# Performance work log

Hardware: AMD Instinct MI355X
Metric: run time of the kernel (lower is better)

Reference implementation:

```python
import jax, jax.numpy as jnp
import numpy as np

V, E, CIN, COUT, NH, HID = 8192, 2048, 128, 128, 4, 32
EPS = 1e-5

def _ln(x, g, b):
    m = x.mean(-1, keepdims=True)
    v = x.var(-1, keepdims=True)
    return (x - m) / jnp.sqrt(v + EPS) * g + b

def setup_inputs() -> dict:
    key = jax.random.key(0)
    ks = jax.random.split(key, 12)
    s = 0.05
    X = jax.random.normal(ks[0], (V, CIN), jnp.float32)
    H = jax.random.bernoulli(ks[1], 0.02, (V, E)).astype(jnp.float32)
    edge_features = jax.random.normal(ks[2], (E, COUT), jnp.float32)
    Wv = jax.random.normal(ks[3], (CIN, COUT), jnp.float32) * s
    bv = jnp.zeros((COUT,), jnp.float32)
    We = jax.random.normal(ks[4], (COUT, COUT), jnp.float32) * s
    be = jnp.zeros((COUT,), jnp.float32)
    vW1 = jax.random.normal(ks[5], (NH, CIN, HID), jnp.float32) * s
    vb1 = jnp.zeros((NH, HID), jnp.float32)
    vW2 = jax.random.normal(ks[6], (NH, HID), jnp.float32) * s
    vb2 = jnp.zeros((NH,), jnp.float32)
    eW1 = jax.random.normal(ks[7], (COUT, HID), jnp.float32) * s
    eb1 = jnp.zeros((HID,), jnp.float32)
    eW2 = jax.random.normal(ks[8], (HID,), jnp.float32) * s
    eb2 = jnp.zeros((), jnp.float32)
    Wc = jax.random.normal(ks[9], (NH * COUT, COUT), jnp.float32) * s
    bc = jnp.zeros((COUT,), jnp.float32)
    Wg = jax.random.normal(ks[10], (CIN + COUT, COUT), jnp.float32) * s
    bg = jnp.zeros((COUT,), jnp.float32)
    return dict(X=X, H=H, edge_features=edge_features, Wv=Wv, bv=bv, We=We, be=be,
                vW1=vW1, vb1=vb1, vW2=vW2, vb2=vb2, eW1=eW1, eb1=eb1, eW2=eW2, eb2=eb2,
                Wc=Wc, bc=bc,
                ln_e_g=jnp.ones((COUT,), jnp.float32), ln_e_b=jnp.zeros((COUT,), jnp.float32),
                ln_v_g=jnp.ones((COUT,), jnp.float32), ln_v_b=jnp.zeros((COUT,), jnp.float32),
                bn_g=jnp.ones((COUT,), jnp.float32), bn_b=jnp.zeros((COUT,), jnp.float32),
                Wg=Wg, bg=bg)

def reference(X, H, edge_features, Wv, bv, We, be, vW1, vb1, vW2, vb2,
              eW1, eb1, eW2, eb2, Wc, bc, ln_e_g, ln_e_b, ln_v_g, ln_v_b,
              bn_g, bn_b, Wg, bg):
    gelu = lambda t: jax.nn.gelu(t, approximate=False)  # torch nn.GELU default (erf)
    Ht = H.T                                   # (E, V)
    Xt = X @ Wv + bv                           # (V, Cout) theta_v
    # per-head vertex attention MLP: Linear(Cin,32)->GELU->Linear(32,1), vectorized over heads
    hid = gelu(jnp.einsum('vc,hck->hvk', X, vW1) + vb1[:, None, :])
    attn = jax.nn.sigmoid(jnp.einsum('hvk,hk->hv', hid, vW2) + vb2[:, None])  # (NH, V)
    deg = Ht.sum(axis=1, keepdims=True)        # (E, 1) edge degrees
    denom = jnp.maximum(deg, 1.0)
    # degree-normalized attention-weighted v2e aggregation per head
    head_e = jnp.einsum('ev,hvc->hec', Ht, Xt[None] * attn[:, :, None]) / denom[None]
    e_cat = jnp.transpose(head_e, (1, 0, 2)).reshape(E, NH * COUT)  # concat heads dim=1
    e_feat = e_cat @ Wc + bc                   # attn_combine
    # edge attention uses the LAST head's vertex weights (global-var quirk in torch code)
    edge_att = ((Ht @ attn[-1]) / jnp.maximum(deg[:, 0], 1.0))[:, None]  # (E,1)
    # edge-feature gating with e_attention head 0
    te = edge_features @ We + be               # theta_e
    e_scores = gelu(e_feat @ eW1 + eb1) @ eW2 + eb2
    ew = jax.nn.sigmoid(e_scores)[:, None]
    e_feat = e_feat * ew + te * (1.0 - ew)
    # normalize == 'both': layer_norm_e then batch_norm (training-mode batch stats)
    e_feat = _ln(e_feat, ln_e_g, ln_e_b)
    m = e_feat.mean(axis=0)
    v = e_feat.var(axis=0)
    e_feat = (e_feat - m) / jnp.sqrt(v + EPS) * bn_g + bn_b
    # e2v sum aggregation: H @ e_feat
    v_feat = H @ e_feat                        # (V, Cout)
    gate = jax.nn.sigmoid(jnp.concatenate([X, v_feat], axis=1) @ Wg + bg)
    v_feat = gate * v_feat + (1.0 - gate) * Xt
    v_feat = _ln(v_feat, ln_v_g, ln_v_b)
    v_feat = v_feat + X                        # residual (Cin == Cout)
    v_feat = gelu(v_feat)                      # not is_last: activation; dropout = identity (eval)
    e_feat = gelu(e_feat)
    return v_feat, e_feat, edge_att
```

## Files before the change

### kernel.cpp

```cpp
#include <hip/hip_runtime.h>
#include <hip/hip_bf16.h>
#include <math.h>

#define NV 8192
#define NE 2048
#define CIN 128
#define COUT 128
#define NH 4
#define HID 32
#define EPB 4
#define LCAP 256
#define VCAP 96
#define NWORDS (NE / 64)
#define TWORDS (NV / 64)
#define EPSV 1e-5f

__device__ __forceinline__ float gelu_f(float x) {
    return 0.5f * x * (1.0f + erff(x * 0.70710678118654752f));
}
__device__ __forceinline__ float sigmoid_f(float x) {
    return 1.0f / (1.0f + expf(-x));
}

__global__ __launch_bounds__(128) void k_vertex1(
    const float* __restrict__ X, const float* __restrict__ Wv, const float* __restrict__ bv,
    const float* __restrict__ vW1, const float* __restrict__ vb1,
    const float* __restrict__ vW2, const float* __restrict__ vb2,
    float* __restrict__ Xt, float* __restrict__ attn4)
{
    const int VPB = 8;
    __shared__ float Xs[VPB][CIN];
    int t = threadIdx.x;
    int v0 = blockIdx.x * VPB;
    for (int v = 0; v < VPB; ++v) Xs[v][t] = X[(v0 + v) * CIN + t];
    __syncthreads();

    float acc[VPB];
    float bvc = bv[t];
#pragma unroll
    for (int v = 0; v < VPB; ++v) acc[v] = bvc;
    for (int k = 0; k < CIN; ++k) {
        float w = Wv[k * COUT + t];
#pragma unroll
        for (int v = 0; v < VPB; ++v) acc[v] = fmaf(Xs[v][k], w, acc[v]);
    }
    for (int v = 0; v < VPB; ++v) Xt[(v0 + v) * COUT + t] = acc[v];

    int h = t >> 5, j = t & 31;
    float hb = vb1[h * HID + j];
#pragma unroll
    for (int v = 0; v < VPB; ++v) acc[v] = hb;
    for (int k = 0; k < CIN; ++k) {
        float w = vW1[(h * CIN + k) * HID + j];
#pragma unroll
        for (int v = 0; v < VPB; ++v) acc[v] = fmaf(Xs[v][k], w, acc[v]);
    }
    float w2 = vW2[h * HID + j];
    float b2 = vb2[h];
    for (int v = 0; v < VPB; ++v) {
        float val = gelu_f(acc[v]) * w2;
#pragma unroll
        for (int m = 16; m >= 1; m >>= 1) val += __shfl_xor(val, m, 64);
        if (j == 0) attn4[(v0 + v) * NH + h] = sigmoid_f(val + b2);
    }
}

__global__ __launch_bounds__(256) void k_build(
    const float* __restrict__ H, unsigned long long* __restrict__ Hbits,
    int* __restrict__ vdeg, int* __restrict__ vlist)
{
    int w = threadIdx.x >> 6;
    int lane = threadIdx.x & 63;
    int v = blockIdx.x * 4 + w;
    const float* row = H + (size_t)v * NE;
    unsigned long long lt = (1ull << lane) - 1ull;
    int base = 0;
    int* vl = vlist + (size_t)v * VCAP;
#pragma unroll 8
    for (int it = 0; it < NWORDS; ++it) {
        float hv = row[it * 64 + lane];
        bool nz = hv != 0.0f;
        unsigned long long m = __ballot(nz);
        if (lane == 0) Hbits[(size_t)v * NWORDS + it] = m;
        if (nz) {
            int pos = base + __popcll(m & lt);
            if (pos < VCAP) vl[pos] = it * 64 + lane;
        }
        base += __popcll(m);
    }
    if (lane == 0) vdeg[v] = base;
}

__global__ __launch_bounds__(256) void k_transpose(
    const unsigned long long* __restrict__ Hbits, unsigned long long* __restrict__ HbitsT)
{
    __shared__ unsigned long long rows[64][NWORDS];
    int t = threadIdx.x;
    int vt = blockIdx.x;
    for (int i = t; i < 64 * NWORDS; i += 256)
        rows[i >> 5][i & 31] = Hbits[(size_t)vt * 64 * NWORDS + i];
    __syncthreads();
    int wv = t >> 6;
    int lane = t & 63;
    const unsigned long long M[6] = {
        0xFFFFFFFF00000000ULL, 0xFFFF0000FFFF0000ULL, 0xFF00FF00FF00FF00ULL,
        0xF0F0F0F0F0F0F0F0ULL, 0xCCCCCCCCCCCCCCCCULL, 0xAAAAAAAAAAAAAAAAULL };
    const int js[6] = {32, 16, 8, 4, 2, 1};
#pragma unroll
    for (int itb = 0; itb < 8; ++itb) {
        int it = wv * 8 + itb;
        unsigned long long x = rows[lane][it];
#pragma unroll
        for (int s = 0; s < 6; ++s) {
            int j = js[s];
            unsigned long long y = __shfl_xor(x, j, 64);
            unsigned long long Ms = M[s];
            if ((lane & j) == 0) x = (x & ~Ms) | ((y << j) & Ms);
            else                 x = (x & Ms) | ((y >> j) & ~Ms);
        }
        HbitsT[(size_t)(it * 64 + lane) * TWORDS + vt] = x;
    }
}

__global__ __launch_bounds__(512) void k_edge(
    const float* __restrict__ Xt, const float* __restrict__ attn4,
    const unsigned long long* __restrict__ HbitsT,
    const float* __restrict__ edge_features,
    const float* __restrict__ Wc, const float* __restrict__ bc,
    const float* __restrict__ We, const float* __restrict__ be,
    const float* __restrict__ eW1, const float* __restrict__ eb1,
    const float* __restrict__ eW2, const float* __restrict__ eb2,
    const float* __restrict__ ln_g, const float* __restrict__ ln_b,
    float* __restrict__ e_ln, float* __restrict__ out_att)
{
    __shared__ int lst[EPB][LCAP];
    __shared__ int wsum[EPB][2];
    __shared__ float ecat[EPB][NH * COUT];
    __shared__ float efpart[4][EPB * COUT];
    __shared__ float tepart[4][EPB * COUT];
    __shared__ float efr_s[EPB][COUT];
    __shared__ float efs[EPB][COUT];
    __shared__ float teL[EPB][COUT];
    __shared__ float ews[EPB];
    __shared__ float red[EPB][2][2];

    int t = threadIdx.x;
    int g = t >> 7;
    int c = t & 127;
    int lane = t & 63;
    int gw = (t >> 6) & 1;
    int e0 = blockIdx.x * EPB;
    int e = e0 + g;

    efr_s[g][c] = edge_features[(size_t)e * COUT + c];

    unsigned long long wd = HbitsT[(size_t)e * TWORDS + c];
    int cntT = __popcll(wd);
    int inc = cntT;
#pragma unroll
    for (int s = 1; s < 64; s <<= 1) {
        int y = __shfl_up(inc, s, 64);
        if (lane >= s) inc += y;
    }
    if (lane == 63) wsum[g][gw] = inc;
    __syncthreads();
    int base = (gw ? wsum[g][0] : 0) + inc - cntT;
    int n0 = wsum[g][0] + wsum[g][1];
    int vbase = c * 64;
    unsigned long long mm = wd;
    while (mm) {
        int i = __ffsll(mm) - 1;
        mm &= mm - 1;
        if (base < LCAP) lst[g][base] = vbase + i;
        ++base;
    }
    __syncthreads();

    float inv = 1.0f / fmaxf((float)n0, 1.0f);
    int n = n0 < LCAP ? n0 : LCAP;

    float a0 = 0, a1 = 0, a2 = 0, a3 = 0, as = 0;
    for (int i = 0; i < n; ++i) {
        int v = lst[g][i];
        float x = Xt[(size_t)v * COUT + c];
        float4 a = *(const float4*)(attn4 + (size_t)v * NH);
        a0 = fmaf(x, a.x, a0);
        a1 = fmaf(x, a.y, a1);
        a2 = fmaf(x, a.z, a2);
        a3 = fmaf(x, a.w, a3);
        as += a.w;
    }
    ecat[g][0 * COUT + c] = a0 * inv;
    ecat[g][1 * COUT + c] = a1 * inv;
    ecat[g][2 * COUT + c] = a2 * inv;
    ecat[g][3 * COUT + c] = a3 * inv;
    if (c == 0) out_att[e] = as * inv;
    __syncthreads();

    {
        float accW[EPB] = {0, 0, 0, 0};
        const float* wp = Wc + (size_t)(g * 128) * COUT + c;
        for (int k = 0; k < 128; ++k) {
            float w = wp[k * COUT];
#pragma unroll
            for (int ee = 0; ee < EPB; ++ee)
                accW[ee] = fmaf(ecat[ee][g * 128 + k], w, accW[ee]);
        }
#pragma unroll
        for (int ee = 0; ee < EPB; ++ee) efpart[g][ee * COUT + c] = accW[ee];

        float accT[EPB] = {0, 0, 0, 0};
        const float* wt = We + (size_t)(g * 32) * COUT + c;
        for (int k = 0; k < 32; ++k) {
            float w = wt[k * COUT];
#pragma unroll
            for (int ee = 0; ee < EPB; ++ee)
                accT[ee] = fmaf(efr_s[ee][g * 32 + k], w, accT[ee]);
        }
#pragma unroll
        for (int ee = 0; ee < EPB; ++ee) tepart[g][ee * COUT + c] = accT[ee];
    }
    __syncthreads();

    {
        float ef = efpart[0][g * COUT + c] + efpart[1][g * COUT + c]
                 + efpart[2][g * COUT + c] + efpart[3][g * COUT + c] + bc[c];
        float te = tepart[0][g * COUT + c] + tepart[1][g * COUT + c]
                 + tepart[2][g * COUT + c] + tepart[3][g * COUT + c] + be[c];
        efs[g][c] = ef;
        teL[g][c] = te;
    }
    __syncthreads();

    if (t < 128) {
        int ee = t >> 5, j = t & 31;
        float hj = eb1[j];
        for (int k = 0; k < COUT; ++k) hj = fmaf(efs[ee][k], eW1[k * HID + j], hj);
        float val = gelu_f(hj) * eW2[j];
#pragma unroll
        for (int m = 16; m >= 1; m >>= 1) val += __shfl_xor(val, m, 32);
        if ((t & 31) == 0) ews[ee] = sigmoid_f(val + eb2[0]);
    }
    __syncthreads();

    {
        float ew = ews[g];
        float x = efs[g][c] * ew + teL[g][c] * (1.0f - ew);
        float s = x, q = x * x;
#pragma unroll
        for (int m = 32; m >= 1; m >>= 1) { s += __shfl_xor(s, m, 64); q += __shfl_xor(q, m, 64); }
        if (lane == 0) { red[g][gw][0] = s; red[g][gw][1] = q; }
        __syncthreads();
        float S = red[g][0][0] + red[g][1][0];
        float Q = red[g][0][1] + red[g][1][1];
        float m = S * (1.0f / COUT);
        float var = Q * (1.0f / COUT) - m * m;
        float y = (x - m) * rsqrtf(var + EPSV) * ln_g[c] + ln_b[c];
        e_ln[(size_t)e * COUT + c] = y;
    }
}

__global__ __launch_bounds__(128) void k_bnstats(const float* __restrict__ e_ln,
    float* __restrict__ bn_sum, float* __restrict__ bn_sq)
{
    int c = threadIdx.x;
    int e0 = blockIdx.x * 16;
    float s = 0, q = 0;
    for (int i = 0; i < 16; ++i) {
        float x = e_ln[(e0 + i) * COUT + c];
        s += x;
        q += x * x;
    }
    atomicAdd(&bn_sum[c], s);
    atomicAdd(&bn_sq[c], q);
}

__global__ __launch_bounds__(256) void k_bnapply(const float* __restrict__ e_ln,
    const float* __restrict__ bn_sum, const float* __restrict__ bn_sq,
    const float* __restrict__ bn_g, const float* __restrict__ bn_b,
    float* __restrict__ e_n, float* __restrict__ out_e)
{
    int idx = blockIdx.x * 256 + threadIdx.x;
    int c = idx & 127;
    float m = bn_sum[c] * (1.0f / NE);
    float var = bn_sq[c] * (1.0f / NE) - m * m;
    float x = e_ln[idx];
    float y = (x - m) * rsqrtf(var + EPSV) * bn_g[c] + bn_b[c];
    e_n[idx] = y;
    out_e[idx] = gelu_f(y);
}

__global__ __launch_bounds__(512) void k_vertex2(
    const float* __restrict__ X, const int* __restrict__ vdeg, const int* __restrict__ vlist,
    const float* __restrict__ e_n, const float* __restrict__ Xt,
    const float* __restrict__ Wg, const float* __restrict__ bg,
    const float* __restrict__ ln_g, const float* __restrict__ ln_b,
    float* __restrict__ out_v)
{
    __shared__ float Xs[4][CIN];
    __shared__ float vf[4][COUT];
    __shared__ int lst[4][VCAP];
    __shared__ int degs[4];
    __shared__ float red[8][2];
    int t = threadIdx.x;
    int g = t >> 7, c = t & 127;
    int wid = t >> 6;
    int v0 = blockIdx.x * 4;
    int v = v0 + g;

    Xs[g][c] = X[(size_t)v * CIN + c];
    if (c < VCAP) lst[g][c] = vlist[(size_t)v * VCAP + c];
    if (t < 4) degs[t] = vdeg[v0 + t];
    __syncthreads();

    int n = degs[g];
    if (n > VCAP) n = VCAP;
    float acc = 0;
    for (int i = 0; i < n; ++i) acc += e_n[lst[g][i] * COUT + c];
    vf[g][c] = acc;
    __syncthreads();

    float ag = bg[c];
    for (int k = 0; k < CIN; ++k) ag = fmaf(Xs[g][k], Wg[k * COUT + c], ag);
    for (int k = 0; k < COUT; ++k) ag = fmaf(vf[g][k], Wg[(CIN + k) * COUT + c], ag);

    float gate = sigmoid_f(ag);
    float xt = Xt[(size_t)v * COUT + c];
    float x = gate * vf[g][c] + (1.0f - gate) * xt;
    float s = x, q = x * x;
#pragma unroll
    for (int m = 32; m >= 1; m >>= 1) { s += __shfl_xor(s, m, 64); q += __shfl_xor(q, m, 64); }
    if ((t & 63) == 0) { red[wid][0] = s; red[wid][1] = q; }
    __syncthreads();
    float S = red[g * 2][0] + red[g * 2 + 1][0];
    float Q = red[g * 2][1] + red[g * 2 + 1][1];
    float m_ = S * (1.0f / COUT);
    float var = Q * (1.0f / COUT) - m_ * m_;
    float y = (x - m_) * rsqrtf(var + EPSV) * ln_g[c] + ln_b[c];
    y = y + Xs[g][c];
    out_v[(size_t)v * COUT + c] = gelu_f(y);
}

extern "C" void kernel_launch(void* const* d_in, const int* in_sizes, int n_in,
                              void* d_out, int out_size, void* d_ws, size_t ws_size,
                              hipStream_t stream) {
    const float* X    = (const float*)d_in[0];
    const float* H    = (const float*)d_in[1];
    const float* edge_features = (const float*)d_in[2];
    const float* Wv   = (const float*)d_in[3];
    const float* bv   = (const float*)d_in[4];
    const float* We   = (const float*)d_in[5];
    const float* be   = (const float*)d_in[6];
    const float* vW1  = (const float*)d_in[7];
    const float* vb1  = (const float*)d_in[8];
    const float* vW2  = (const float*)d_in[9];
    const float* vb2  = (const float*)d_in[10];
    const float* eW1  = (const float*)d_in[11];
    const float* eb1  = (const float*)d_in[12];
    const float* eW2  = (const float*)d_in[13];
    const float* eb2  = (const float*)d_in[14];
    const float* Wc   = (const float*)d_in[15];
    const float* bc   = (const float*)d_in[16];
    const float* ln_e_g = (const float*)d_in[17];
    const float* ln_e_b = (const float*)d_in[18];
    const float* ln_v_g = (const float*)d_in[19];
    const float* ln_v_b = (const float*)d_in[20];
    const float* bn_g = (const float*)d_in[21];
    const float* bn_b = (const float*)d_in[22];
    const float* Wg   = (const float*)d_in[23];
    const float* bg   = (const float*)d_in[24];

    float* out_v  = (float*)d_out;
    float* out_e  = out_v + NV * COUT;
    float* out_att = out_e + NE * COUT;

    char* w = (char*)d_ws;
    float* Xt     = (float*)w; w += (size_t)NV * COUT * 4;
    float* attn4  = (float*)w; w += (size_t)NV * NH * 4;
    float* e_ln   = (float*)w; w += (size_t)NE * COUT * 4;
    float* e_n    = (float*)w; w += (size_t)NE * COUT * 4;
    float* bn_sum = (float*)w; w += COUT * 4;
    float* bn_sq  = (float*)w; w += COUT * 4;
    int*   vdeg   = (int*)w;   w += (size_t)NV * 4;
    int*   vlist  = (int*)w;   w += (size_t)NV * VCAP * 4;
    unsigned long long* Hbits  = (unsigned long long*)w; w += (size_t)NV * NWORDS * 8;
    unsigned long long* HbitsT = (unsigned long long*)w; w += (size_t)NE * TWORDS * 8;

    hipMemsetAsync(bn_sum, 0, 2 * COUT * sizeof(float), stream);

    k_vertex1<<<NV / 8, 128, 0, stream>>>(X, Wv, bv, vW1, vb1, vW2, vb2, Xt, attn4);
    k_build<<<NV / 4, 256, 0, stream>>>(H, Hbits, vdeg, vlist);
    k_transpose<<<NV / 64, 256, 0, stream>>>(Hbits, HbitsT);
    k_edge<<<NE / EPB, 512, 0, stream>>>(Xt, attn4, HbitsT, edge_features,
                                         Wc, bc, We, be, eW1, eb1, eW2, eb2,
                                         ln_e_g, ln_e_b, e_ln, out_att);
    k_bnstats<<<NE / 16, 128, 0, stream>>>(e_ln, bn_sum, bn_sq);
    k_bnapply<<<(NE * COUT) / 256, 256, 0, stream>>>(e_ln, bn_sum, bn_sq, bn_g, bn_b, e_n, out_e);
    k_vertex2<<<NV / 4, 512, 0, stream>>>(X, vdeg, vlist, e_n, Xt, Wg, bg, ln_v_g, ln_v_b, out_v);
}
```

Measured before the change: 285.8 us.

## Fuse front kernels, fold BN stats into edge kernel and BN affine into vertex gather

Merges the vertex projection and the incidence-bitmask build into one launch using block-index branching. It also accumulates batch-norm statistics inside the edge kernel, which removes the separate stats kernel. The vertex kernel now gathers the pre-BN edge features and applies the BN affine algebraically (A*sum + n*B), so the normalized edge buffer no longer needs to be written and read. It also reworks the edge gather so each wave handles half the vertex list over all 128 channels, and the vertex kernel processes 8 vertices per block with a split-K gate matmul. In exchange it adds more shared memory per block, extra syncs and heavier per-block register use.

```diff
diff --git a/kernel.cpp b/kernel.cpp
--- a/kernel.cpp
+++ b/kernel.cpp
@@ -22,73 +22,73 @@
     return 1.0f / (1.0f + expf(-x));
 }
 
-__global__ __launch_bounds__(128) void k_vertex1(
+__global__ __launch_bounds__(256) void k_front(
     const float* __restrict__ X, const float* __restrict__ Wv, const float* __restrict__ bv,
     const float* __restrict__ vW1, const float* __restrict__ vb1,
     const float* __restrict__ vW2, const float* __restrict__ vb2,
-    float* __restrict__ Xt, float* __restrict__ attn4)
+    const float* __restrict__ H,
+    float* __restrict__ Xt, float* __restrict__ attn4,
+    unsigned long long* __restrict__ Hbits, int* __restrict__ vdeg, int* __restrict__ vlist)
 {
-    const int VPB = 8;
-    __shared__ float Xs[VPB][CIN];
+    __shared__ float Xs[2][8][CIN];
     int t = threadIdx.x;
-    int v0 = blockIdx.x * VPB;
-    for (int v = 0; v < VPB; ++v) Xs[v][t] = X[(v0 + v) * CIN + t];
-    __syncthreads();
-
-    float acc[VPB];
-    float bvc = bv[t];
-#pragma unroll
-    for (int v = 0; v < VPB; ++v) acc[v] = bvc;
-    for (int k = 0; k < CIN; ++k) {
-        float w = Wv[k * COUT + t];
-#pragma unroll
-        for (int v = 0; v < VPB; ++v) acc[v] = fmaf(Xs[v][k], w, acc[v]);
-    }
-    for (int v = 0; v < VPB; ++v) Xt[(v0 + v) * COUT + t] = acc[v];
-
-    int h = t >> 5, j = t & 31;
-    float hb = vb1[h * HID + j];
-#pragma unroll
-    for (int v = 0; v < VPB; ++v) acc[v] = hb;
-    for (int k = 0; k < CIN; ++k) {
-        float w = vW1[(h * CIN + k) * HID + j];
-#pragma unroll
-        for (int v = 0; v < VPB; ++v) acc[v] = fmaf(Xs[v][k], w, acc[v]);
-    }
-    float w2 = vW2[h * HID + j];
-    float b2 = vb2[h];
-    for (int v = 0; v < VPB; ++v) {
-        float val = gelu_f(acc[v]) * w2;
-#pragma unroll
-        for (int m = 16; m >= 1; m >>= 1) val += __shfl_xor(val, m, 64);
-        if (j == 0) attn4[(v0 + v) * NH + h] = sigmoid_f(val + b2);
-    }
-}
-
-__global__ __launch_bounds__(256) void k_build(
-    const float* __restrict__ H, unsigned long long* __restrict__ Hbits,
-    int* __restrict__ vdeg, int* __restrict__ vlist)
-{
-    int w = threadIdx.x >> 6;
-    int lane = threadIdx.x & 63;
-    int v = blockIdx.x * 4 + w;
-    const float* row = H + (size_t)v * NE;
-    unsigned long long lt = (1ull << lane) - 1ull;
-    int base = 0;
-    int* vl = vlist + (size_t)v * VCAP;
+    if (blockIdx.x < NV / 16) {
+        int half = t >> 7, tt = t & 127;
+        int v0 = blockIdx.x * 16 + half * 8;
+        for (int v = 0; v < 8; ++v) Xs[half][v][tt] = X[(size_t)(v0 + v) * CIN + tt];
+        __syncthreads();
+
+        float acc[8];
+        float bvc = bv[tt];
+#pragma unroll
+        for (int v = 0; v < 8; ++v) acc[v] = bvc;
+        for (int k = 0; k < CIN; ++k) {
+            float w = Wv[k * COUT + tt];
+#pragma unroll
+            for (int v = 0; v < 8; ++v) acc[v] = fmaf(Xs[half][v][k], w, acc[v]);
+        }
+        for (int v = 0; v < 8; ++v) Xt[(size_t)(v0 + v) * COUT + tt] = acc[v];
+
+        int h = tt >> 5, j = tt & 31;
+        float hb = vb1[h * HID + j];
+#pragma unroll
+        for (int v = 0; v < 8; ++v) acc[v] = hb;
+        for (int k = 0; k < CIN; ++k) {
+            float w = vW1[(h * CIN + k) * HID + j];
+#pragma unroll
+            for (int v = 0; v < 8; ++v) acc[v] = fmaf(Xs[half][v][k], w, acc[v]);
+        }
+        float w2 = vW2[h * HID + j];
+        float b2 = vb2[h];
+        for (int v = 0; v < 8; ++v) {
+            float val = gelu_f(acc[v]) * w2;
+#pragma unroll
+            for (int m = 16; m >= 1; m >>= 1) val += __shfl_xor(val, m, 64);
+            if (j == 0) attn4[(size_t)(v0 + v) * NH + h] = sigmoid_f(val + b2);
+        }
+    } else {
+        int b = blockIdx.x - NV / 16;
+        int w = t >> 6;
+        int lane = t & 63;
+        int v = b * 4 + w;
+        const float* row = H + (size_t)v * NE;
+        unsigned long long lt = (1ull << lane) - 1ull;
+        int base = 0;
+        int* vl = vlist + (size_t)v * VCAP;
 #pragma unroll 8
-    for (int it = 0; it < NWORDS; ++it) {
-        float hv = row[it * 64 + lane];
-        bool nz = hv != 0.0f;
-        unsigned long long m = __ballot(nz);
-        if (lane == 0) Hbits[(size_t)v * NWORDS + it] = m;
-        if (nz) {
-            int pos = base + __popcll(m & lt);
-            if (pos < VCAP) vl[pos] = it * 64 + lane;
-        }
-        base += __popcll(m);
-    }
-    if (lane == 0) vdeg[v] = base;
+        for (int it = 0; it < NWORDS; ++it) {
+            float hv = row[it * 64 + lane];
+            bool nz = hv != 0.0f;
+            unsigned long long m = __ballot(nz);
+            if (lane == 0) Hbits[(size_t)v * NWORDS + it] = m;
+            if (nz) {
+                int pos = base + __popcll(m & lt);
+                if (pos < VCAP) vl[pos] = it * 64 + lane;
+            }
+            base += __popcll(m);
+        }
+        if (lane == 0) vdeg[v] = base;
+    }
 }
 
 __global__ __launch_bounds__(256) void k_transpose(
@@ -131,17 +131,18 @@
     const float* __restrict__ eW1, const float* __restrict__ eb1,
     const float* __restrict__ eW2, const float* __restrict__ eb2,
     const float* __restrict__ ln_g, const float* __restrict__ ln_b,
-    float* __restrict__ e_ln, float* __restrict__ out_att)
+    float* __restrict__ e_ln, float* __restrict__ out_att,
+    float* __restrict__ bn_sum, float* __restrict__ bn_sq)
 {
     __shared__ int lst[EPB][LCAP];
     __shared__ int wsum[EPB][2];
+    __shared__ float scratch[4096];
     __shared__ float ecat[EPB][NH * COUT];
-    __shared__ float efpart[4][EPB * COUT];
-    __shared__ float tepart[4][EPB * COUT];
     __shared__ float efr_s[EPB][COUT];
     __shared__ float efs[EPB][COUT];
     __shared__ float teL[EPB][COUT];
     __shared__ float ews[EPB];
+    __shared__ float asp[EPB][2];
     __shared__ float red[EPB][2][2];
 
     int t = threadIdx.x;
@@ -149,8 +150,7 @@
     int c = t & 127;
     int lane = t & 63;
     int gw = (t >> 6) & 1;
-    int e0 = blockIdx.x * EPB;
-    int e = e0 + g;
+    int e = blockIdx.x * EPB + g;
 
     efr_s[g][c] = edge_features[(size_t)e * COUT + c];
 
@@ -179,22 +179,36 @@
     float inv = 1.0f / fmaxf((float)n0, 1.0f);
     int n = n0 < LCAP ? n0 : LCAP;
 
-    float a0 = 0, a1 = 0, a2 = 0, a3 = 0, as = 0;
-    for (int i = 0; i < n; ++i) {
+    float p00 = 0, p10 = 0, p20 = 0, p30 = 0;
+    float p01 = 0, p11 = 0, p21 = 0, p31 = 0;
+    float as = 0;
+    for (int i = gw; i < n; i += 2) {
         int v = lst[g][i];
-        float x = Xt[(size_t)v * COUT + c];
+        float x0 = Xt[(size_t)v * COUT + lane];
+        float x1 = Xt[(size_t)v * COUT + lane + 64];
         float4 a = *(const float4*)(attn4 + (size_t)v * NH);
-        a0 = fmaf(x, a.x, a0);
-        a1 = fmaf(x, a.y, a1);
-        a2 = fmaf(x, a.z, a2);
-        a3 = fmaf(x, a.w, a3);
+        p00 = fmaf(x0, a.x, p00);  p01 = fmaf(x1, a.x, p01);
+        p10 = fmaf(x0, a.y, p10);  p11 = fmaf(x1, a.y, p11);
+        p20 = fmaf(x0, a.z, p20);  p21 = fmaf(x1, a.z, p21);
+        p30 = fmaf(x0, a.w, p30);  p31 = fmaf(x1, a.w, p31);
         as += a.w;
     }
-    ecat[g][0 * COUT + c] = a0 * inv;
-    ecat[g][1 * COUT + c] = a1 * inv;
-    ecat[g][2 * COUT + c] = a2 * inv;
-    ecat[g][3 * COUT + c] = a3 * inv;
-    if (c == 0) out_att[e] = as * inv;
+    {
+        int bi = (g * 2 + gw) * NH * COUT;
+        scratch[bi + 0 * COUT + lane] = p00;  scratch[bi + 0 * COUT + lane + 64] = p01;
+        scratch[bi + 1 * COUT + lane] = p10;  scratch[bi + 1 * COUT + lane + 64] = p11;
+        scratch[bi + 2 * COUT + lane] = p20;  scratch[bi + 2 * COUT + lane + 64] = p21;
+        scratch[bi + 3 * COUT + lane] = p30;  scratch[bi + 3 * COUT + lane + 64] = p31;
+    }
+    if (lane == 0) asp[g][gw] = as;
+    __syncthreads();
+
+#pragma unroll
+    for (int h = 0; h < NH; ++h)
+        ecat[g][h * COUT + c] =
+            (scratch[(g * 2 + 0) * NH * COUT + h * COUT + c] +
+             scratch[(g * 2 + 1) * NH * COUT + h * COUT + c]) * inv;
+    if (c == 0) out_att[e] = (asp[g][0] + asp[g][1]) * inv;
     __syncthreads();
 
     {
@@ -207,7 +221,7 @@
                 accW[ee] = fmaf(ecat[ee][g * 128 + k], w, accW[ee]);
         }
 #pragma unroll
-        for (int ee = 0; ee < EPB; ++ee) efpart[g][ee * COUT + c] = accW[ee];
+        for (int ee = 0; ee < EPB; ++ee) scratch[g * 512 + ee * COUT + c] = accW[ee];
 
         float accT[EPB] = {0, 0, 0, 0};
         const float* wt = We + (size_t)(g * 32) * COUT + c;
@@ -218,18 +232,14 @@
                 accT[ee] = fmaf(efr_s[ee][g * 32 + k], w, accT[ee]);
         }
 #pragma unroll
-        for (int ee = 0; ee < EPB; ++ee) tepart[g][ee * COUT + c] = accT[ee];
-    }
-    __syncthreads();
-
-    {
-        float ef = efpart[0][g * COUT + c] + efpart[1][g * COUT + c]
-                 + efpart[2][g * COUT + c] + efpart[3][g * COUT + c] + bc[c];
-        float te = tepart[0][g * COUT + c] + tepart[1][g * COUT + c]
-                 + tepart[2][g * COUT + c] + tepart[3][g * COUT + c] + be[c];
-        efs[g][c] = ef;
-        teL[g][c] = te;
-    }
+        for (int ee = 0; ee < EPB; ++ee) scratch[2048 + g * 512 + ee * COUT + c] = accT[ee];
+    }
+    __syncthreads();
+
+    efs[g][c] = scratch[0 * 512 + g * COUT + c] + scratch[1 * 512 + g * COUT + c]
+              + scratch[2 * 512 + g * COUT + c] + scratch[3 * 512 + g * COUT + c] + bc[c];
+    teL[g][c] = scratch[2048 + 0 * 512 + g * COUT + c] + scratch[2048 + 1 * 512 + g * COUT + c]
+              + scratch[2048 + 2 * 512 + g * COUT + c] + scratch[2048 + 3 * 512 + g * COUT + c] + be[c];
     __syncthreads();
 
     if (t < 128) {
@@ -243,6 +253,7 @@
     }
     __syncthreads();
 
+    float y;
     {
         float ew = ews[g];
         float x = efs[g][c] * ew + teL[g][c] * (1.0f - ew);
@@ -255,30 +266,24 @@
         float Q = red[g][0][1] + red[g][1][1];
         float m = S * (1.0f / COUT);
         float var = Q * (1.0f / COUT) - m * m;
-        float y = (x - m) * rsqrtf(var + EPSV) * ln_g[c] + ln_b[c];
+        y = (x - m) * rsqrtf(var + EPSV) * ln_g[c] + ln_b[c];
         e_ln[(size_t)e * COUT + c] = y;
     }
-}
-
-__global__ __launch_bounds__(128) void k_bnstats(const float* __restrict__ e_ln,
-    float* __restrict__ bn_sum, float* __restrict__ bn_sq)
-{
-    int c = threadIdx.x;
-    int e0 = blockIdx.x * 16;
-    float s = 0, q = 0;
-    for (int i = 0; i < 16; ++i) {
-        float x = e_ln[(e0 + i) * COUT + c];
-        s += x;
-        q += x * x;
-    }
-    atomicAdd(&bn_sum[c], s);
-    atomicAdd(&bn_sq[c], q);
+    scratch[g * COUT + c] = y;
+    scratch[512 + g * COUT + c] = y * y;
+    __syncthreads();
+    if (t < 128) {
+        float s = scratch[t] + scratch[COUT + t] + scratch[2 * COUT + t] + scratch[3 * COUT + t];
+        float q = scratch[512 + t] + scratch[512 + COUT + t] + scratch[512 + 2 * COUT + t] + scratch[512 + 3 * COUT + t];
+        atomicAdd(&bn_sum[t], s);
+        atomicAdd(&bn_sq[t], q);
+    }
 }
 
 __global__ __launch_bounds__(256) void k_bnapply(const float* __restrict__ e_ln,
     const float* __restrict__ bn_sum, const float* __restrict__ bn_sq,
     const float* __restrict__ bn_g, const float* __restrict__ bn_b,
-    float* __restrict__ e_n, float* __restrict__ out_e)
+    float* __restrict__ out_e)
 {
     int idx = blockIdx.x * 256 + threadIdx.x;
     int c = idx & 127;
@@ -286,59 +291,105 @@
     float var = bn_sq[c] * (1.0f / NE) - m * m;
     float x = e_ln[idx];
     float y = (x - m) * rsqrtf(var + EPSV) * bn_g[c] + bn_b[c];
-    e_n[idx] = y;
     out_e[idx] = gelu_f(y);
 }
 
 __global__ __launch_bounds__(512) void k_vertex2(
     const float* __restrict__ X, const int* __restrict__ vdeg, const int* __restrict__ vlist,
-    const float* __restrict__ e_n, const float* __restrict__ Xt,
+    const float* __restrict__ e_ln,
+    const float* __restrict__ bn_sum, const float* __restrict__ bn_sq,
+    const float* __restrict__ bn_g, const float* __restrict__ bn_b,
+    const float* __restrict__ Xt,
     const float* __restrict__ Wg, const float* __restrict__ bg,
     const float* __restrict__ ln_g, const float* __restrict__ ln_b,
     float* __restrict__ out_v)
 {
-    __shared__ float Xs[4][CIN];
-    __shared__ float vf[4][COUT];
-    __shared__ int lst[4][VCAP];
-    __shared__ int degs[4];
-    __shared__ float red[8][2];
+    __shared__ float XsF[8 * CIN];
+    __shared__ float vfF[8 * COUT];
+    __shared__ int lst[8][VCAP];
+    __shared__ int degs[8];
+    __shared__ float part[4 * 8 * COUT];
+    __shared__ float red[8][2][2];
+
     int t = threadIdx.x;
-    int g = t >> 7, c = t & 127;
-    int wid = t >> 6;
-    int v0 = blockIdx.x * 4;
-    int v = v0 + g;
-
-    Xs[g][c] = X[(size_t)v * CIN + c];
-    if (c < VCAP) lst[g][c] = vlist[(size_t)v * VCAP + c];
-    if (t < 4) degs[t] = vdeg[v0 + t];
-    __syncthreads();
-
-    int n = degs[g];
+    int vg = t >> 6, lane = t & 63;
+    int g4 = t >> 7, c = t & 127;
+    int gw2 = (t >> 6) & 1;
+    int v0 = blockIdx.x * 8;
+
+    {
+        float2 x2 = *(const float2*)(X + (size_t)(v0 + vg) * CIN + lane * 2);
+        XsF[vg * CIN + lane * 2] = x2.x;
+        XsF[vg * CIN + lane * 2 + 1] = x2.y;
+    }
+    for (int i = t; i < 8 * VCAP; i += 512)
+        lst[i / VCAP][i % VCAP] = vlist[(size_t)v0 * VCAP + i];
+    if (t < 8) degs[t] = vdeg[v0 + t];
+    __syncthreads();
+
+    int ch0 = lane * 2;
+    float m0 = bn_sum[ch0] * (1.0f / NE);
+    float m1 = bn_sum[ch0 + 1] * (1.0f / NE);
+    float A0 = bn_g[ch0] * rsqrtf(bn_sq[ch0] * (1.0f / NE) - m0 * m0 + EPSV);
+    float A1 = bn_g[ch0 + 1] * rsqrtf(bn_sq[ch0 + 1] * (1.0f / NE) - m1 * m1 + EPSV);
+    float B0 = bn_b[ch0] - m0 * A0;
+    float B1 = bn_b[ch0 + 1] - m1 * A1;
+
+    int n = degs[vg];
     if (n > VCAP) n = VCAP;
-    float acc = 0;
-    for (int i = 0; i < n; ++i) acc += e_n[lst[g][i] * COUT + c];
-    vf[g][c] = acc;
-    __syncthreads();
-
-    float ag = bg[c];
-    for (int k = 0; k < CIN; ++k) ag = fmaf(Xs[g][k], Wg[k * COUT + c], ag);
-    for (int k = 0; k < COUT; ++k) ag = fmaf(vf[g][k], Wg[(CIN + k) * COUT + c], ag);
-
-    float gate = sigmoid_f(ag);
-    float xt = Xt[(size_t)v * COUT + c];
-    float x = gate * vf[g][c] + (1.0f - gate) * xt;
-    float s = x, q = x * x;
-#pragma unroll
-    for (int m = 32; m >= 1; m >>= 1) { s += __shfl_xor(s, m, 64); q += __shfl_xor(q, m, 64); }
-    if ((t & 63) == 0) { red[wid][0] = s; red[wid][1] = q; }
-    __syncthreads();
-    float S = red[g * 2][0] + red[g * 2 + 1][0];
-    float Q = red[g * 2][1] + red[g * 2 + 1][1];
-    float m_ = S * (1.0f / COUT);
-    float var = Q * (1.0f / COUT) - m_ * m_;
-    float y = (x - m_) * rsqrtf(var + EPSV) * ln_g[c] + ln_b[c];
-    y = y + Xs[g][c];
-    out_v[(size_t)v * COUT + c] = gelu_f(y);
+    float sx = 0, sy = 0;
+    for (int i = 0; i < n; ++i) {
+        float2 v2 = *(const float2*)(e_ln + (size_t)lst[vg][i] * COUT + ch0);
+        sx += v2.x;
+        sy += v2.y;
+    }
+    float fn = (float)n;
+    vfF[vg * COUT + ch0] = A0 * sx + fn * B0;
+    vfF[vg * COUT + ch0 + 1] = A1 * sy + fn * B1;
+    __syncthreads();
+
+    {
+        float accW[8] = {0, 0, 0, 0, 0, 0, 0, 0};
+        const float* wp = Wg + (size_t)(g4 * 64) * COUT + c;
+        const float* src = (g4 < 2) ? XsF : vfF;
+        int kb = (g4 & 1) * 64;
+        for (int ki = 0; ki < 64; ++ki) {
+            float w = wp[(size_t)ki * COUT];
+#pragma unroll
+            for (int v = 0; v < 8; ++v)
+                accW[v] = fmaf(src[v * 128 + kb + ki], w, accW[v]);
+        }
+#pragma unroll
+        for (int v = 0; v < 8; ++v) part[g4 * 1024 + v * COUT + c] = accW[v];
+    }
+    __syncthreads();
+
+    float xv[2];
+#pragma unroll
+    for (int rep = 0; rep < 2; ++rep) {
+        int v = g4 + rep * 4;
+        float ag = part[0 * 1024 + v * COUT + c] + part[1 * 1024 + v * COUT + c]
+                 + part[2 * 1024 + v * COUT + c] + part[3 * 1024 + v * COUT + c] + bg[c];
+        float gate = sigmoid_f(ag);
+        float x = gate * vfF[v * COUT + c] + (1.0f - gate) * Xt[(size_t)(v0 + v) * COUT + c];
+        xv[rep] = x;
+        float s = x, q = x * x;
+#pragma unroll
+        for (int m = 32; m >= 1; m >>= 1) { s += __shfl_xor(s, m, 64); q += __shfl_xor(q, m, 64); }
+        if (lane == 0) { red[v][gw2][0] = s; red[v][gw2][1] = q; }
+    }
+    __syncthreads();
+#pragma unroll
+    for (int rep = 0; rep < 2; ++rep) {
+        int v = g4 + rep * 4;
+        float S = red[v][0][0] + red[v][1][0];
+        float Q = red[v][0][1] + red[v][1][1];
+        float m_ = S * (1.0f / COUT);
+        float var = Q * (1.0f / COUT) - m_ * m_;
+        float y = (xv[rep] - m_) * rsqrtf(var + EPSV) * ln_g[c] + ln_b[c];
+        y = y + XsF[v * CIN + c];
+        out_v[(size_t)(v0 + v) * COUT + c] = gelu_f(y);
+    }
 }
 
 extern "C" void kernel_launch(void* const* d_in, const int* in_sizes, int n_in,
@@ -378,7 +429,6 @@
     float* Xt     = (float*)w; w += (size_t)NV * COUT * 4;
     float* attn4  = (float*)w; w += (size_t)NV * NH * 4;
     float* e_ln   = (float*)w; w += (size_t)NE * COUT * 4;
-    float* e_n    = (float*)w; w += (size_t)NE * COUT * 4;
     float* bn_sum = (float*)w; w += COUT * 4;
     float* bn_sq  = (float*)w; w += COUT * 4;
     int*   vdeg   = (int*)w;   w += (size_t)NV * 4;
@@ -388,13 +438,13 @@
 
     hipMemsetAsync(bn_sum, 0, 2 * COUT * sizeof(float), stream);
 
-    k_vertex1<<<NV / 8, 128, 0, stream>>>(X, Wv, bv, vW1, vb1, vW2, vb2, Xt, attn4);
-    k_build<<<NV / 4, 256, 0, stream>>>(H, Hbits, vdeg, vlist);
+    k_front<<<NV / 16 + NV / 4, 256, 0, stream>>>(X, Wv, bv, vW1, vb1, vW2, vb2, H,
+                                                  Xt, attn4, Hbits, vdeg, vlist);
     k_transpose<<<NV / 64, 256, 0, stream>>>(Hbits, HbitsT);
     k_edge<<<NE / EPB, 512, 0, stream>>>(Xt, attn4, HbitsT, edge_features,
                                          Wc, bc, We, be, eW1, eb1, eW2, eb2,
-                                         ln_e_g, ln_e_b, e_ln, out_att);
-    k_bnstats<<<NE / 16, 128, 0, stream>>>(e_ln, bn_sum, bn_sq);
-    k_bnapply<<<(NE * COUT) / 256, 256, 0, stream>>>(e_ln, bn_sum, bn_sq, bn_g, bn_b, e_n, out_e);
-    k_vertex2<<<NV / 4, 512, 0, stream>>>(X, vdeg, vlist, e_n, Xt, Wg, bg, ln_v_g, ln_v_b, out_v);
-}
+                                         ln_e_g, ln_e_b, e_ln, out_att, bn_sum, bn_sq);
+    k_bnapply<<<(NE * COUT) / 256, 256, 0, stream>>>(e_ln, bn_sum, bn_sq, bn_g, bn_b, out_e);
+    k_vertex2<<<NV / 8, 512, 0, stream>>>(X, vdeg, vlist, e_ln, bn_sum, bn_sq, bn_g, bn_b,
+                                          Xt, Wg, bg, ln_v_g, ln_v_b, out_v);
+}
```

Measured after the change: 263.6 us. 1.08x faster.
